# Optimization experiments

Measured on AMD Instinct MI355X. Metric: run time of the kernel, lower is better.

The kernel has to match this reference:

```python
import jax, jax.numpy as jnp
import numpy as np

B, IN, LAT, HID, OUT = 1024, 256, 512, 1024, 64
N_STEPS = 20          # fixed-step RK4 stand-in for adaptive odeint
T0, T1 = 0.0, 1.0     # integration interval from `time=(0.0, 1.0)`


def setup_inputs() -> dict:
    key = jax.random.key(0)
    ks = jax.random.split(key, 6)
    def glorot(k, shape):
        fan = shape[0]
        return (jax.random.normal(k, shape, jnp.float32) / np.float32(np.sqrt(fan)))
    return {
        "x": jax.random.normal(ks[0], (B, IN), jnp.float32),
        "W_in": glorot(ks[1], (IN, LAT)),
        "b_in": jnp.zeros((LAT,), jnp.float32),
        "W1": glorot(ks[2], (LAT + 1, HID)),   # +1 for the time column
        "b1": jnp.zeros((HID,), jnp.float32),
        "W2": glorot(ks[3], (HID, LAT)),
        "b2": jnp.zeros((LAT,), jnp.float32),
        "W_out": glorot(ks[4], (LAT // 2, OUT)),
        "b_out": jnp.zeros((OUT,), jnp.float32),
    }


def reference(x, W_in, b_in, W1, b1, W2, b2, W_out, b_out):
    # dynamics(inputs, time): concat scalar time as extra feature, run MLP
    def dyn(h, t):
        t_col = t * jnp.ones((h.shape[0], 1), h.dtype)
        z = jnp.concatenate([h, t_col], axis=-1)          # [B, LAT+1]
        return jnp.tanh(z @ W1 + b1) @ W2 + b2            # [B, LAT]

    # input_net: Dense + tanh
    h0 = jnp.tanh(x @ W_in + b_in)                        # [B, LAT]

    dt = jnp.float32((T1 - T0) / N_STEPS)
    ts = T0 + dt * jnp.arange(N_STEPS, dtype=jnp.float32)

    def rk4_step(h, t):
        k1 = dyn(h, t)
        k2 = dyn(h + 0.5 * dt * k1, t + 0.5 * dt)
        k3 = dyn(h + 0.5 * dt * k2, t + 0.5 * dt)
        k4 = dyn(h + dt * k3, t + dt)
        return h + (dt / 6.0) * (k1 + 2.0 * k2 + 2.0 * k3 + k4), None

    hT, _ = jax.lax.scan(rk4_step, h0, ts)                # latent at t=T1

    hidden = hT[:, : LAT // 2]                            # first half of latent
    out = hidden @ W_out + b_out                          # outputs head
    return out
```

## Files before the change

### kernel.cpp

```cpp
#include <hip/hip_runtime.h>
#include <hip/hip_bf16.h>

typedef __bf16 bf16x8 __attribute__((ext_vector_type(8)));
typedef __bf16 bf16x4 __attribute__((ext_vector_type(4)));
typedef float  f32x4  __attribute__((ext_vector_type(4)));

static constexpr int BB   = 1024;
static constexpr int INF  = 256;
static constexpr int LATF = 512;
static constexpr int HIDF = 1024;
static constexpr int OUTF = 64;
static constexpr float DT = 0.05f;

__device__ __forceinline__ void gload_lds16(const __bf16* g, __bf16* l) {
    __builtin_amdgcn_global_load_lds(
        (const __attribute__((address_space(1))) void*)g,
        (__attribute__((address_space(3))) void*)l, 16, 0, 0);
}

__device__ __forceinline__ void gload_lds16_x(const __bf16* g, __bf16* l, bool l2) {
    if (l2)
        __builtin_amdgcn_global_load_lds(
            (const __attribute__((address_space(1))) void*)g,
            (__attribute__((address_space(3))) void*)l, 16, 0, 1);
    else
        __builtin_amdgcn_global_load_lds(
            (const __attribute__((address_space(1))) void*)g,
            (__attribute__((address_space(3))) void*)l, 16, 0, 17);
}

__device__ __forceinline__ void store_bf16_x(__bf16* p, float v, bool l2) {
    const __bf16 b = (__bf16)v;
    unsigned u;
    __builtin_memcpy(&u, &b, 2);
    if (l2)
        asm volatile("global_store_short %0, %1, off sc0" :: "v"(p), "v"(u) : "memory");
    else
        asm volatile("global_store_short %0, %1, off sc0 sc1" :: "v"(p), "v"(u) : "memory");
}

__device__ __forceinline__ void drain_vmem() {
    asm volatile("s_waitcnt vmcnt(0)" ::: "memory");
}

__device__ __forceinline__ unsigned atomic_peek_l2(unsigned* p) {
    unsigned v, zero = 0;
    asm volatile("global_atomic_add %0, %1, %2, off sc0\n\ts_waitcnt vmcnt(0)"
                 : "=v"(v) : "v"(p), "v"(zero) : "memory");
    return v;
}

__device__ __forceinline__ void post_x(unsigned* p, bool l2) {
    if (l2) {
        unsigned one = 1u;
        asm volatile("global_atomic_add %0, %1, off" :: "v"(p), "v"(one) : "memory");
    } else {
        __hip_atomic_fetch_add(p, 1u, __ATOMIC_RELAXED, __HIP_MEMORY_SCOPE_AGENT);
    }
}

__device__ __forceinline__ void spin_ge_t0(unsigned* p, unsigned tgt, bool l2) {
    int guard = 0;
    if (l2) {
        while (atomic_peek_l2(p) < tgt) {
            __builtin_amdgcn_s_sleep(1);
            if (++guard > (1 << 16)) break;
        }
    } else {
        while (__hip_atomic_load(p, __ATOMIC_RELAXED, __HIP_MEMORY_SCOPE_AGENT) < tgt) {
            __builtin_amdgcn_s_sleep(1);
            if (++guard > (1 << 22)) break;
        }
    }
}

__device__ __forceinline__ float tanh_fast(float x) {
    float e = __expf(2.0f * x);
    return (e - 1.0f) / (e + 1.0f);
}

__global__ __launch_bounds__(256)
void prep_k(const float* __restrict__ x, __bf16* __restrict__ xb,
            const float* __restrict__ W_in, __bf16* __restrict__ WinT,
            const float* __restrict__ W1, __bf16* __restrict__ W1T,
            const float* __restrict__ W2, __bf16* __restrict__ W2T) {
    const int b = blockIdx.x;
    const int tx = threadIdx.x, ty = threadIdx.y;
    if (b < 256) {
        const int i = b * 256 + ty * 32 + tx;
        float4 v = reinterpret_cast<const float4*>(x)[i];
        bf16x4 o;
        o[0] = (__bf16)v.x; o[1] = (__bf16)v.y; o[2] = (__bf16)v.z; o[3] = (__bf16)v.w;
        reinterpret_cast<bf16x4*>(xb)[i] = o;
        return;
    }
    const float* src; __bf16* dst; int R, C, tb;
    if (b < 384)      { src = W_in; dst = WinT; R = 256;  C = 512;  tb = b - 256; }
    else if (b < 896) { src = W1;   dst = W1T;  R = 512;  C = 1024; tb = b - 384; }
    else              { src = W2;   dst = W2T;  R = 1024; C = 512;  tb = b - 896; }
    __shared__ float tile[32][33];
    const int nbc = C / 32;
    const int c0 = (tb % nbc) * 32, r0 = (tb / nbc) * 32;
#pragma unroll
    for (int i = 0; i < 32; i += 8)
        tile[ty + i][tx] = src[(size_t)(r0 + ty + i) * C + (c0 + tx)];
    __syncthreads();
#pragma unroll
    for (int i = 0; i < 32; i += 8)
        dst[(size_t)(c0 + ty + i) * R + (r0 + tx)] = (__bf16)tile[tx][ty + i];
}

__global__ __launch_bounds__(256, 1)
void ode_persist(const __bf16* __restrict__ xb, const __bf16* __restrict__ WinT,
                 const __bf16* __restrict__ W1T, const __bf16* __restrict__ W2T,
                 const float* __restrict__ b_in, const float* __restrict__ b1,
                 const float* __restrict__ wlast, const float* __restrict__ b2,
                 __bf16* __restrict__ zG, __bf16* __restrict__ gG,
                 float* __restrict__ hG, unsigned* __restrict__ flags) {
    __shared__ __align__(16) unsigned char SL[65536];
    __shared__ int sh_l2ok;

    const int bid   = blockIdx.x;
    const int rb    = (bid & 7) * 4 + ((bid >> 3) & 3);
    const int slice = bid >> 5;
    const int r0 = rb * 32;
    const int c1 = slice * 128;
    const int c2 = slice * 64;

    unsigned* czp = flags + rb * 32;
    unsigned* cgp = flags + rb * 32 + 16;

    const int tid  = threadIdx.x;
    const int w    = tid >> 6;
    const int lane = tid & 63;
    const int fr   = lane & 15;
    const int kq   = lane >> 4;
    const int cw   = w & 1;
    const int kw   = w >> 1;

    if (tid == 0) {
        unsigned* cvp   = flags + 1024;
        unsigned* cvp2  = flags + 1056;
        unsigned* trial = flags + 2048 + rb * 32;
        unsigned* vis   = flags + 4096;
        unsigned* okb   = flags + 12288;
        const unsigned magic = 0xC0DE0000u | (unsigned)bid;
        asm volatile("global_store_dword %0, %1, off sc0" :: "v"(&vis[bid * 32]), "v"(magic) : "memory");
        drain_vmem();
        __hip_atomic_fetch_add(cvp, 1u, __ATOMIC_RELAXED, __HIP_MEMORY_SCOPE_AGENT);
        { int g = 0; while (__hip_atomic_load(cvp, __ATOMIC_RELAXED, __HIP_MEMORY_SCOPE_AGENT) < 256u) { __builtin_amdgcn_s_sleep(1); if (++g > (1 << 22)) break; } }
        unsigned ok = 1;
        for (int s = 0; s < 8; ++s) {
            const int pb = (rb >> 2) + 8 * (rb & 3) + 32 * s;
            unsigned v;
            asm volatile("global_load_dword %0, %1, off sc0\n\ts_waitcnt vmcnt(0)"
                         : "=v"(v) : "v"(&vis[pb * 32]) : "memory");
            ok &= (v == (0xC0DE0000u | (unsigned)pb)) ? 1u : 0u;
        }
        {
            unsigned one = 1u;
            asm volatile("global_atomic_add %0, %1, off" :: "v"(trial), "v"(one) : "memory");
            int g = 0;
            while (atomic_peek_l2(trial) < 8u) {
                __builtin_amdgcn_s_sleep(1);
                if (++g > (1 << 15)) { ok = 0; break; }
            }
        }
        asm volatile("global_store_dword %0, %1, off sc0 sc1" :: "v"(&okb[bid * 32]), "v"(ok) : "memory");
        drain_vmem();
        __hip_atomic_fetch_add(cvp2, 1u, __ATOMIC_RELAXED, __HIP_MEMORY_SCOPE_AGENT);
        { int g = 0; while (__hip_atomic_load(cvp2, __ATOMIC_RELAXED, __HIP_MEMORY_SCOPE_AGENT) < 256u) { __builtin_amdgcn_s_sleep(1); if (++g > (1 << 22)) break; } }
        unsigned allok = 1;
        for (int s = 0; s < 8; ++s) {
            const int pb = (rb >> 2) + 8 * (rb & 3) + 32 * s;
            unsigned v;
            asm volatile("global_load_dword %0, %1, off sc0 sc1\n\ts_waitcnt vmcnt(0)"
                         : "=v"(v) : "v"(&okb[pb * 32]) : "memory");
            allok &= v;
        }
        sh_l2ok = (int)allok;
    }
    __syncthreads();
    const bool l2m = (sh_l2ok != 0);

    bf16x8 b1r[2][16];
#pragma unroll
    for (int n = 0; n < 2; ++n)
#pragma unroll
        for (int ks = 0; ks < 16; ++ks)
            b1r[n][ks] = *reinterpret_cast<const bf16x8*>(
                W1T + (size_t)(c1 + 32 * w + 16 * n + fr) * 512 + ks * 32 + kq * 8);

    bf16x8 b2r[2][16];
#pragma unroll
    for (int n = 0; n < 2; ++n)
#pragma unroll
        for (int ks = 0; ks < 16; ++ks)
            b2r[n][ks] = *reinterpret_cast<const bf16x8*>(
                W2T + (size_t)(c2 + 32 * cw + 16 * n + fr) * 1024 + kw * 512 + ks * 32 + kq * 8);

    float b1v[2], wlv[2], b2v[2], binv[2];
#pragma unroll
    for (int n = 0; n < 2; ++n) {
        const int colg = c1 + 32 * w + 16 * n + fr;
        b1v[n] = b1[colg];
        wlv[n] = wlast[colg];
        const int colk = c2 + 32 * cw + 16 * n + fr;
        b2v[n] = b2[colk];
        binv[n] = b_in[colk];
    }

    f32x4 hr[2][2], ha[2][2];

    {
#pragma unroll
        for (int i = 0; i < 4; ++i) {
            const int idx = w * 4 + i;
            const int row = idx * 2 + (lane >> 5);
            const int gam = (lane & 31) ^ (row & 7);
            gload_lds16(xb + (size_t)(r0 + row) * 256 + gam * 8,
                        (__bf16*)(SL + (size_t)idx * 1024));
        }
        bf16x8 winr[2][4];
#pragma unroll
        for (int n = 0; n < 2; ++n)
#pragma unroll
            for (int ks = 0; ks < 4; ++ks)
                winr[n][ks] = *reinterpret_cast<const bf16x8*>(
                    WinT + (size_t)(c2 + 32 * cw + 16 * n + fr) * 256 + kw * 128 + ks * 32 + kq * 8);
        __syncthreads();

        f32x4 acc[2][2];
#pragma unroll
        for (int mi = 0; mi < 2; ++mi)
#pragma unroll
            for (int n = 0; n < 2; ++n) acc[mi][n] = f32x4{0.f, 0.f, 0.f, 0.f};
#pragma unroll
        for (int ks = 0; ks < 4; ++ks) {
            bf16x8 a[2];
#pragma unroll
            for (int mi = 0; mi < 2; ++mi) {
                const int rowA = 16 * mi + fr;
                const int gk = kw * 16 + ks * 4 + kq;
                a[mi] = *reinterpret_cast<const bf16x8*>(
                    SL + (size_t)rowA * 512 + ((gk ^ (rowA & 7)) << 4));
            }
#pragma unroll
            for (int mi = 0; mi < 2; ++mi)
#pragma unroll
                for (int n = 0; n < 2; ++n)
                    acc[mi][n] = __builtin_amdgcn_mfma_f32_16x16x32_bf16(a[mi], winr[n][ks],
                                                                         acc[mi][n], 0, 0, 0);
        }
        __syncthreads();
        if (kw == 1) {
#pragma unroll
            for (int mi = 0; mi < 2; ++mi)
#pragma unroll
                for (int n = 0; n < 2; ++n)
                    *reinterpret_cast<f32x4*>(SL + cw * 4096 + ((mi * 2 + n) * 64 + lane) * 16) =
                        acc[mi][n];
        }
        __syncthreads();
        if (kw == 0) {
#pragma unroll
            for (int mi = 0; mi < 2; ++mi)
#pragma unroll
                for (int n = 0; n < 2; ++n) {
                    f32x4 part = *reinterpret_cast<const f32x4*>(
                        SL + cw * 4096 + ((mi * 2 + n) * 64 + lane) * 16);
#pragma unroll
                    for (int j = 0; j < 4; ++j) {
                        const float v = tanh_fast(acc[mi][n][j] + part[j] + binv[n]);
                        hr[mi][n][j] = v;
                        store_bf16_x(zG + (size_t)(r0 + 16 * mi + kq * 4 + j) * 512 +
                                          (c2 + 32 * cw + 16 * n + fr), v, l2m);
                    }
                }
        }
        drain_vmem();
        __syncthreads();
        if (tid == 0) post_x(czp, l2m);
    }

    for (int it = 0; it < 80; ++it) {
        const int s4 = it >> 2, st = it & 3;
        const float t = DT * (float)s4 + ((st == 0) ? 0.f : (st == 3) ? DT : 0.5f * DT);
        const unsigned tgt = 8u * (unsigned)(it + 1);

        if (tid == 0) spin_ge_t0(czp, tgt, l2m);
        __syncthreads();
#pragma unroll
        for (int i = 0; i < 8; ++i) {
            const int row = w * 8 + i;
            const int gam = lane ^ (row & 7);
            gload_lds16_x(zG + (size_t)(r0 + row) * 512 + gam * 8,
                          (__bf16*)(SL + (size_t)row * 1024), l2m);
        }
        __syncthreads();
        {
            f32x4 acc[2][2];
#pragma unroll
            for (int mi = 0; mi < 2; ++mi)
#pragma unroll
                for (int n = 0; n < 2; ++n) acc[mi][n] = f32x4{0.f, 0.f, 0.f, 0.f};
#pragma unroll
            for (int ks = 0; ks < 16; ++ks) {
                bf16x8 a[2];
#pragma unroll
                for (int mi = 0; mi < 2; ++mi) {
                    const int rowA = 16 * mi + fr;
                    const int gk = ks * 4 + kq;
                    a[mi] = *reinterpret_cast<const bf16x8*>(
                        SL + (size_t)rowA * 1024 + ((gk ^ (rowA & 7)) << 4));
                }
#pragma unroll
                for (int mi = 0; mi < 2; ++mi)
#pragma unroll
                    for (int n = 0; n < 2; ++n)
                        acc[mi][n] = __builtin_amdgcn_mfma_f32_16x16x32_bf16(a[mi], b1r[n][ks],
                                                                             acc[mi][n], 0, 0, 0);
            }
#pragma unroll
            for (int mi = 0; mi < 2; ++mi)
#pragma unroll
                for (int n = 0; n < 2; ++n)
#pragma unroll
                    for (int j = 0; j < 4; ++j) {
                        const float gv = tanh_fast(acc[mi][n][j] + b1v[n] + t * wlv[n]);
                        store_bf16_x(gG + (size_t)(r0 + 16 * mi + kq * 4 + j) * 1024 +
                                          (c1 + 32 * w + 16 * n + fr), gv, l2m);
                    }
        }
        drain_vmem();
        __syncthreads();
        if (tid == 0) {
            post_x(cgp, l2m);
            spin_ge_t0(cgp, tgt, l2m);
        }
        __syncthreads();
#pragma unroll
        for (int i = 0; i < 16; ++i) {
            const int idx = w * 16 + i;
            const int row = idx >> 1;
            const int p = ((idx & 1) << 6) | lane;
            const int gam = p ^ (row & 7);
            gload_lds16_x(gG + (size_t)(r0 + row) * 1024 + gam * 8,
                          (__bf16*)(SL + (size_t)idx * 1024), l2m);
        }
        __syncthreads();
        {
            f32x4 acc[2][2];
#pragma unroll
            for (int mi = 0; mi < 2; ++mi)
#pragma unroll
                for (int n = 0; n < 2; ++n) acc[mi][n] = f32x4{0.f, 0.f, 0.f, 0.f};
#pragma unroll
            for (int ks = 0; ks < 16; ++ks) {
                bf16x8 a[2];
#pragma unroll
                for (int mi = 0; mi < 2; ++mi) {
                    const int rowA = 16 * mi + fr;
                    const int gk = kw * 64 + ks * 4 + kq;
                    a[mi] = *reinterpret_cast<const bf16x8*>(
                        SL + (size_t)rowA * 2048 + ((gk ^ (rowA & 7)) << 4));
                }
#pragma unroll
                for (int mi = 0; mi < 2; ++mi)
#pragma unroll
                    for (int n = 0; n < 2; ++n)
                        acc[mi][n] = __builtin_amdgcn_mfma_f32_16x16x32_bf16(a[mi], b2r[n][ks],
                                                                             acc[mi][n], 0, 0, 0);
            }
            __syncthreads();
            if (kw == 1) {
#pragma unroll
                for (int mi = 0; mi < 2; ++mi)
#pragma unroll
                    for (int n = 0; n < 2; ++n)
                        *reinterpret_cast<f32x4*>(SL + cw * 4096 + ((mi * 2 + n) * 64 + lane) * 16) =
                            acc[mi][n];
            }
            __syncthreads();
            if (kw == 0) {
                const float wA = (st == 0 || st == 3) ? (DT / 6.0f) : (DT / 3.0f);
                const float cZ = (st < 2) ? (0.5f * DT) : DT;
#pragma unroll
                for (int mi = 0; mi < 2; ++mi)
#pragma unroll
                    for (int n = 0; n < 2; ++n) {
                        f32x4 part = *reinterpret_cast<const f32x4*>(
                            SL + cw * 4096 + ((mi * 2 + n) * 64 + lane) * 16);
#pragma unroll
                        for (int j = 0; j < 4; ++j) {
                            const float kv = acc[mi][n][j] + part[j] + b2v[n];
                            float zv;
                            if (st == 0) {
                                ha[mi][n][j] = hr[mi][n][j] + wA * kv;
                                zv = hr[mi][n][j] + cZ * kv;
                            } else if (st < 3) {
                                ha[mi][n][j] += wA * kv;
                                zv = hr[mi][n][j] + cZ * kv;
                            } else {
                                hr[mi][n][j] = ha[mi][n][j] + wA * kv;
                                zv = hr[mi][n][j];
                            }
                            store_bf16_x(zG + (size_t)(r0 + 16 * mi + kq * 4 + j) * 512 +
                                              (c2 + 32 * cw + 16 * n + fr), zv, l2m);
                        }
                    }
            }
        }
        drain_vmem();
        __syncthreads();
        if (tid == 0) post_x(czp, l2m);
    }

    if (kw == 0) {
#pragma unroll
        for (int mi = 0; mi < 2; ++mi)
#pragma unroll
            for (int n = 0; n < 2; ++n)
#pragma unroll
                for (int j = 0; j < 4; ++j)
                    hG[(size_t)(r0 + 16 * mi + kq * 4 + j) * 512 +
                       (c2 + 32 * cw + 16 * n + fr)] = hr[mi][n][j];
    }
}

__global__ __launch_bounds__(256)
void out_k(const float* __restrict__ h, const float* __restrict__ Wout,
           const float* __restrict__ bout, float* __restrict__ out) {
    const int col = threadIdx.x & 63;
    const int rg  = threadIdx.x >> 6;
    const int r0  = blockIdx.x * 16 + rg * 4;
    float a0 = 0.f, a1 = 0.f, a2 = 0.f, a3 = 0.f;
    for (int k = 0; k < 256; ++k) {
        const float w = Wout[k * OUTF + col];
        a0 += h[(r0 + 0) * LATF + k] * w;
        a1 += h[(r0 + 1) * LATF + k] * w;
        a2 += h[(r0 + 2) * LATF + k] * w;
        a3 += h[(r0 + 3) * LATF + k] * w;
    }
    const float b = bout[col];
    out[(r0 + 0) * OUTF + col] = a0 + b;
    out[(r0 + 1) * OUTF + col] = a1 + b;
    out[(r0 + 2) * OUTF + col] = a2 + b;
    out[(r0 + 3) * OUTF + col] = a3 + b;
}

extern "C" void kernel_launch(void* const* d_in, const int* in_sizes, int n_in,
                              void* d_out, int out_size, void* d_ws, size_t ws_size,
                              hipStream_t stream) {
    const float* x     = (const float*)d_in[0];
    const float* W_in  = (const float*)d_in[1];
    const float* b_in  = (const float*)d_in[2];
    const float* W1    = (const float*)d_in[3];
    const float* b1    = (const float*)d_in[4];
    const float* W2    = (const float*)d_in[5];
    const float* b2    = (const float*)d_in[6];
    const float* W_out = (const float*)d_in[7];
    const float* b_out = (const float*)d_in[8];
    float* out = (float*)d_out;

    char* ws = (char*)d_ws;
    size_t off = 0;
    auto alloc = [&](size_t bytes) {
        void* p = ws + off;
        off += (bytes + 255) & ~(size_t)255;
        return p;
    };
    __bf16* xb   = (__bf16*)alloc((size_t)BB * INF * 2);
    __bf16* WinT = (__bf16*)alloc((size_t)LATF * INF * 2);
    __bf16* W1T  = (__bf16*)alloc((size_t)HIDF * LATF * 2);
    __bf16* W2T  = (__bf16*)alloc((size_t)LATF * HIDF * 2);
    float*  h    = (float*)alloc((size_t)BB * LATF * 4);
    __bf16* zbuf = (__bf16*)alloc((size_t)BB * LATF * 2);
    __bf16* gbuf = (__bf16*)alloc((size_t)BB * HIDF * 2);
    unsigned* flags = (unsigned*)alloc(98304);
    if (off > ws_size) return;

    hipMemsetAsync(flags, 0, 98304, stream);
    prep_k<<<1408, dim3(32, 8), 0, stream>>>(x, xb, W_in, WinT, W1, W1T, W2, W2T);

    const float* w1last = W1 + (size_t)LATF * HIDF;

    ode_persist<<<256, 256, 0, stream>>>(xb, WinT, W1T, W2T, b_in, b1, w1last, b2,
                                         zbuf, gbuf, h, flags);

    out_k<<<BB / 16, 256, 0, stream>>>(h, W_out, b_out, out);
}
```

Baseline: 620.4 us.

## Split persistent ODE kernel into 512 blocks of 16 rows, two per CU

Halves the per-block row tile from 32 to 16 batch rows and doubles the persistent grid to 512 blocks, with launch bounds allowing two blocks per CU and LDS cut to fit. The block-to-row mapping, flag layout, co-residency checks and partner lists are reworked for the larger grid. The aim is more waves per CU to hide latency and shorter per-block critical paths between grid-wide syncs. In exchange each block holds all of its weight slice in registers for only half the rows, so per-row register and weight-load overhead doubles. It also adds register pressure under the tighter launch bound and more synchronisation participants.

```diff
diff --git a/kernel.cpp b/kernel.cpp
--- a/kernel.cpp
+++ b/kernel.cpp
@@ -110,20 +110,20 @@
         dst[(size_t)(c0 + ty + i) * R + (r0 + tx)] = (__bf16)tile[tx][ty + i];
 }
 
-__global__ __launch_bounds__(256, 1)
+__global__ __launch_bounds__(256, 2)
 void ode_persist(const __bf16* __restrict__ xb, const __bf16* __restrict__ WinT,
                  const __bf16* __restrict__ W1T, const __bf16* __restrict__ W2T,
                  const float* __restrict__ b_in, const float* __restrict__ b1,
                  const float* __restrict__ wlast, const float* __restrict__ b2,
                  __bf16* __restrict__ zG, __bf16* __restrict__ gG,
                  float* __restrict__ hG, unsigned* __restrict__ flags) {
-    __shared__ __align__(16) unsigned char SL[65536];
+    __shared__ __align__(16) unsigned char SL[36864];
     __shared__ int sh_l2ok;
 
     const int bid   = blockIdx.x;
-    const int rb    = (bid & 7) * 4 + ((bid >> 3) & 3);
-    const int slice = bid >> 5;
-    const int r0 = rb * 32;
+    const int rb    = (bid & 7) * 8 + ((bid >> 3) & 3) * 2 + (bid >> 8);
+    const int slice = (bid >> 5) & 7;
+    const int r0 = rb * 16;
     const int c1 = slice * 128;
     const int c2 = slice * 64;
 
@@ -139,19 +139,19 @@
     const int kw   = w >> 1;
 
     if (tid == 0) {
-        unsigned* cvp   = flags + 1024;
-        unsigned* cvp2  = flags + 1056;
-        unsigned* trial = flags + 2048 + rb * 32;
-        unsigned* vis   = flags + 4096;
-        unsigned* okb   = flags + 12288;
+        unsigned* cvp   = flags + 2048;
+        unsigned* cvp2  = flags + 2080;
+        unsigned* trial = flags + 4096 + rb * 32;
+        unsigned* vis   = flags + 8192;
+        unsigned* okb   = flags + 24576;
         const unsigned magic = 0xC0DE0000u | (unsigned)bid;
         asm volatile("global_store_dword %0, %1, off sc0" :: "v"(&vis[bid * 32]), "v"(magic) : "memory");
         drain_vmem();
         __hip_atomic_fetch_add(cvp, 1u, __ATOMIC_RELAXED, __HIP_MEMORY_SCOPE_AGENT);
-        { int g = 0; while (__hip_atomic_load(cvp, __ATOMIC_RELAXED, __HIP_MEMORY_SCOPE_AGENT) < 256u) { __builtin_amdgcn_s_sleep(1); if (++g > (1 << 22)) break; } }
+        { int g = 0; while (__hip_atomic_load(cvp, __ATOMIC_RELAXED, __HIP_MEMORY_SCOPE_AGENT) < 512u) { __builtin_amdgcn_s_sleep(1); if (++g > (1 << 22)) break; } }
         unsigned ok = 1;
         for (int s = 0; s < 8; ++s) {
-            const int pb = (rb >> 2) + 8 * (rb & 3) + 32 * s;
+            const int pb = (rb >> 3) | (((rb >> 1) & 3) << 3) | (s << 5) | ((rb & 1) << 8);
             unsigned v;
             asm volatile("global_load_dword %0, %1, off sc0\n\ts_waitcnt vmcnt(0)"
                          : "=v"(v) : "v"(&vis[pb * 32]) : "memory");
@@ -169,10 +169,10 @@
         asm volatile("global_store_dword %0, %1, off sc0 sc1" :: "v"(&okb[bid * 32]), "v"(ok) : "memory");
         drain_vmem();
         __hip_atomic_fetch_add(cvp2, 1u, __ATOMIC_RELAXED, __HIP_MEMORY_SCOPE_AGENT);
-        { int g = 0; while (__hip_atomic_load(cvp2, __ATOMIC_RELAXED, __HIP_MEMORY_SCOPE_AGENT) < 256u) { __builtin_amdgcn_s_sleep(1); if (++g > (1 << 22)) break; } }
+        { int g = 0; while (__hip_atomic_load(cvp2, __ATOMIC_RELAXED, __HIP_MEMORY_SCOPE_AGENT) < 512u) { __builtin_amdgcn_s_sleep(1); if (++g > (1 << 22)) break; } }
         unsigned allok = 1;
         for (int s = 0; s < 8; ++s) {
-            const int pb = (rb >> 2) + 8 * (rb & 3) + 32 * s;
+            const int pb = (rb >> 3) | (((rb >> 1) & 3) << 3) | (s << 5) | ((rb & 1) << 8);
             unsigned v;
             asm volatile("global_load_dword %0, %1, off sc0 sc1\n\ts_waitcnt vmcnt(0)"
                          : "=v"(v) : "v"(&okb[pb * 32]) : "memory");
@@ -210,12 +210,13 @@
         binv[n] = b_in[colk];
     }
 
-    f32x4 hr[2][2], ha[2][2];
+    f32x4 hr[2], ha[2];
+    unsigned char* SCR = SL + 32768;
 
     {
 #pragma unroll
-        for (int i = 0; i < 4; ++i) {
-            const int idx = w * 4 + i;
+        for (int i = 0; i < 2; ++i) {
+            const int idx = w * 2 + i;
             const int row = idx * 2 + (lane >> 5);
             const int gam = (lane & 31) ^ (row & 7);
             gload_lds16(xb + (size_t)(r0 + row) * 256 + gam * 8,
@@ -230,53 +231,37 @@
                     WinT + (size_t)(c2 + 32 * cw + 16 * n + fr) * 256 + kw * 128 + ks * 32 + kq * 8);
         __syncthreads();
 
-        f32x4 acc[2][2];
-#pragma unroll
-        for (int mi = 0; mi < 2; ++mi)
-#pragma unroll
-            for (int n = 0; n < 2; ++n) acc[mi][n] = f32x4{0.f, 0.f, 0.f, 0.f};
+        f32x4 acc[2];
+#pragma unroll
+        for (int n = 0; n < 2; ++n) acc[n] = f32x4{0.f, 0.f, 0.f, 0.f};
 #pragma unroll
         for (int ks = 0; ks < 4; ++ks) {
-            bf16x8 a[2];
-#pragma unroll
-            for (int mi = 0; mi < 2; ++mi) {
-                const int rowA = 16 * mi + fr;
-                const int gk = kw * 16 + ks * 4 + kq;
-                a[mi] = *reinterpret_cast<const bf16x8*>(
-                    SL + (size_t)rowA * 512 + ((gk ^ (rowA & 7)) << 4));
-            }
-#pragma unroll
-            for (int mi = 0; mi < 2; ++mi)
-#pragma unroll
-                for (int n = 0; n < 2; ++n)
-                    acc[mi][n] = __builtin_amdgcn_mfma_f32_16x16x32_bf16(a[mi], winr[n][ks],
-                                                                         acc[mi][n], 0, 0, 0);
+            const int gk = kw * 16 + ks * 4 + kq;
+            bf16x8 a = *reinterpret_cast<const bf16x8*>(
+                SL + (size_t)fr * 512 + ((gk ^ (fr & 7)) << 4));
+#pragma unroll
+            for (int n = 0; n < 2; ++n)
+                acc[n] = __builtin_amdgcn_mfma_f32_16x16x32_bf16(a, winr[n][ks], acc[n], 0, 0, 0);
         }
         __syncthreads();
         if (kw == 1) {
 #pragma unroll
-            for (int mi = 0; mi < 2; ++mi)
-#pragma unroll
-                for (int n = 0; n < 2; ++n)
-                    *reinterpret_cast<f32x4*>(SL + cw * 4096 + ((mi * 2 + n) * 64 + lane) * 16) =
-                        acc[mi][n];
+            for (int n = 0; n < 2; ++n)
+                *reinterpret_cast<f32x4*>(SCR + cw * 2048 + n * 1024 + lane * 16) = acc[n];
         }
         __syncthreads();
         if (kw == 0) {
 #pragma unroll
-            for (int mi = 0; mi < 2; ++mi)
-#pragma unroll
-                for (int n = 0; n < 2; ++n) {
-                    f32x4 part = *reinterpret_cast<const f32x4*>(
-                        SL + cw * 4096 + ((mi * 2 + n) * 64 + lane) * 16);
-#pragma unroll
-                    for (int j = 0; j < 4; ++j) {
-                        const float v = tanh_fast(acc[mi][n][j] + part[j] + binv[n]);
-                        hr[mi][n][j] = v;
-                        store_bf16_x(zG + (size_t)(r0 + 16 * mi + kq * 4 + j) * 512 +
-                                          (c2 + 32 * cw + 16 * n + fr), v, l2m);
-                    }
+            for (int n = 0; n < 2; ++n) {
+                f32x4 part = *reinterpret_cast<const f32x4*>(SCR + cw * 2048 + n * 1024 + lane * 16);
+#pragma unroll
+                for (int j = 0; j < 4; ++j) {
+                    const float v = tanh_fast(acc[n][j] + part[j] + binv[n]);
+                    hr[n][j] = v;
+                    store_bf16_x(zG + (size_t)(r0 + kq * 4 + j) * 512 +
+                                      (c2 + 32 * cw + 16 * n + fr), v, l2m);
                 }
+            }
         }
         drain_vmem();
         __syncthreads();
@@ -291,46 +276,34 @@
         if (tid == 0) spin_ge_t0(czp, tgt, l2m);
         __syncthreads();
 #pragma unroll
-        for (int i = 0; i < 8; ++i) {
-            const int row = w * 8 + i;
+        for (int i = 0; i < 4; ++i) {
+            const int row = w * 4 + i;
             const int gam = lane ^ (row & 7);
             gload_lds16_x(zG + (size_t)(r0 + row) * 512 + gam * 8,
                           (__bf16*)(SL + (size_t)row * 1024), l2m);
         }
         __syncthreads();
         {
-            f32x4 acc[2][2];
-#pragma unroll
-            for (int mi = 0; mi < 2; ++mi)
-#pragma unroll
-                for (int n = 0; n < 2; ++n) acc[mi][n] = f32x4{0.f, 0.f, 0.f, 0.f};
+            f32x4 acc[2];
+#pragma unroll
+            for (int n = 0; n < 2; ++n) acc[n] = f32x4{0.f, 0.f, 0.f, 0.f};
 #pragma unroll
             for (int ks = 0; ks < 16; ++ks) {
-                bf16x8 a[2];
-#pragma unroll
-                for (int mi = 0; mi < 2; ++mi) {
-                    const int rowA = 16 * mi + fr;
-                    const int gk = ks * 4 + kq;
-                    a[mi] = *reinterpret_cast<const bf16x8*>(
-                        SL + (size_t)rowA * 1024 + ((gk ^ (rowA & 7)) << 4));
+                const int gk = ks * 4 + kq;
+                bf16x8 a = *reinterpret_cast<const bf16x8*>(
+                    SL + (size_t)fr * 1024 + ((gk ^ (fr & 7)) << 4));
+#pragma unroll
+                for (int n = 0; n < 2; ++n)
+                    acc[n] = __builtin_amdgcn_mfma_f32_16x16x32_bf16(a, b1r[n][ks], acc[n], 0, 0, 0);
+            }
+#pragma unroll
+            for (int n = 0; n < 2; ++n)
+#pragma unroll
+                for (int j = 0; j < 4; ++j) {
+                    const float gv = tanh_fast(acc[n][j] + b1v[n] + t * wlv[n]);
+                    store_bf16_x(gG + (size_t)(r0 + kq * 4 + j) * 1024 +
+                                      (c1 + 32 * w + 16 * n + fr), gv, l2m);
                 }
-#pragma unroll
-                for (int mi = 0; mi < 2; ++mi)
-#pragma unroll
-                    for (int n = 0; n < 2; ++n)
-                        acc[mi][n] = __builtin_amdgcn_mfma_f32_16x16x32_bf16(a[mi], b1r[n][ks],
-                                                                             acc[mi][n], 0, 0, 0);
-            }
-#pragma unroll
-            for (int mi = 0; mi < 2; ++mi)
-#pragma unroll
-                for (int n = 0; n < 2; ++n)
-#pragma unroll
-                    for (int j = 0; j < 4; ++j) {
-                        const float gv = tanh_fast(acc[mi][n][j] + b1v[n] + t * wlv[n]);
-                        store_bf16_x(gG + (size_t)(r0 + 16 * mi + kq * 4 + j) * 1024 +
-                                          (c1 + 32 * w + 16 * n + fr), gv, l2m);
-                    }
         }
         drain_vmem();
         __syncthreads();
@@ -340,8 +313,8 @@
         }
         __syncthreads();
 #pragma unroll
-        for (int i = 0; i < 16; ++i) {
-            const int idx = w * 16 + i;
+        for (int i = 0; i < 8; ++i) {
+            const int idx = w * 8 + i;
             const int row = idx >> 1;
             const int p = ((idx & 1) << 6) | lane;
             const int gam = p ^ (row & 7);
@@ -350,65 +323,50 @@
         }
         __syncthreads();
         {
-            f32x4 acc[2][2];
-#pragma unroll
-            for (int mi = 0; mi < 2; ++mi)
-#pragma unroll
-                for (int n = 0; n < 2; ++n) acc[mi][n] = f32x4{0.f, 0.f, 0.f, 0.f};
+            f32x4 acc[2];
+#pragma unroll
+            for (int n = 0; n < 2; ++n) acc[n] = f32x4{0.f, 0.f, 0.f, 0.f};
 #pragma unroll
             for (int ks = 0; ks < 16; ++ks) {
-                bf16x8 a[2];
-#pragma unroll
-                for (int mi = 0; mi < 2; ++mi) {
-                    const int rowA = 16 * mi + fr;
-                    const int gk = kw * 64 + ks * 4 + kq;
-                    a[mi] = *reinterpret_cast<const bf16x8*>(
-                        SL + (size_t)rowA * 2048 + ((gk ^ (rowA & 7)) << 4));
-                }
-#pragma unroll
-                for (int mi = 0; mi < 2; ++mi)
-#pragma unroll
-                    for (int n = 0; n < 2; ++n)
-                        acc[mi][n] = __builtin_amdgcn_mfma_f32_16x16x32_bf16(a[mi], b2r[n][ks],
-                                                                             acc[mi][n], 0, 0, 0);
+                const int gk = kw * 64 + ks * 4 + kq;
+                bf16x8 a = *reinterpret_cast<const bf16x8*>(
+                    SL + (size_t)fr * 2048 + ((gk ^ (fr & 7)) << 4));
+#pragma unroll
+                for (int n = 0; n < 2; ++n)
+                    acc[n] = __builtin_amdgcn_mfma_f32_16x16x32_bf16(a, b2r[n][ks], acc[n], 0, 0, 0);
             }
             __syncthreads();
             if (kw == 1) {
 #pragma unroll
-                for (int mi = 0; mi < 2; ++mi)
-#pragma unroll
-                    for (int n = 0; n < 2; ++n)
-                        *reinterpret_cast<f32x4*>(SL + cw * 4096 + ((mi * 2 + n) * 64 + lane) * 16) =
-                            acc[mi][n];
+                for (int n = 0; n < 2; ++n)
+                    *reinterpret_cast<f32x4*>(SCR + cw * 2048 + n * 1024 + lane * 16) = acc[n];
             }
             __syncthreads();
             if (kw == 0) {
                 const float wA = (st == 0 || st == 3) ? (DT / 6.0f) : (DT / 3.0f);
                 const float cZ = (st < 2) ? (0.5f * DT) : DT;
 #pragma unroll
-                for (int mi = 0; mi < 2; ++mi)
-#pragma unroll
-                    for (int n = 0; n < 2; ++n) {
-                        f32x4 part = *reinterpret_cast<const f32x4*>(
-                            SL + cw * 4096 + ((mi * 2 + n) * 64 + lane) * 16);
-#pragma unroll
-                        for (int j = 0; j < 4; ++j) {
-                            const float kv = acc[mi][n][j] + part[j] + b2v[n];
-                            float zv;
-                            if (st == 0) {
-                                ha[mi][n][j] = hr[mi][n][j] + wA * kv;
-                                zv = hr[mi][n][j] + cZ * kv;
-                            } else if (st < 3) {
-                                ha[mi][n][j] += wA * kv;
-                                zv = hr[mi][n][j] + cZ * kv;
-                            } else {
-                                hr[mi][n][j] = ha[mi][n][j] + wA * kv;
-                                zv = hr[mi][n][j];
-                            }
-                            store_bf16_x(zG + (size_t)(r0 + 16 * mi + kq * 4 + j) * 512 +
-                                              (c2 + 32 * cw + 16 * n + fr), zv, l2m);
+                for (int n = 0; n < 2; ++n) {
+                    f32x4 part = *reinterpret_cast<const f32x4*>(
+                        SCR + cw * 2048 + n * 1024 + lane * 16);
+#pragma unroll
+                    for (int j = 0; j < 4; ++j) {
+                        const float kv = acc[n][j] + part[j] + b2v[n];
+                        float zv;
+                        if (st == 0) {
+                            ha[n][j] = hr[n][j] + wA * kv;
+                            zv = hr[n][j] + cZ * kv;
+                        } else if (st < 3) {
+                            ha[n][j] += wA * kv;
+                            zv = hr[n][j] + cZ * kv;
+                        } else {
+                            hr[n][j] = ha[n][j] + wA * kv;
+                            zv = hr[n][j];
                         }
+                        store_bf16_x(zG + (size_t)(r0 + kq * 4 + j) * 512 +
+                                          (c2 + 32 * cw + 16 * n + fr), zv, l2m);
                     }
+                }
             }
         }
         drain_vmem();
@@ -418,13 +376,11 @@
 
     if (kw == 0) {
 #pragma unroll
-        for (int mi = 0; mi < 2; ++mi)
-#pragma unroll
-            for (int n = 0; n < 2; ++n)
-#pragma unroll
-                for (int j = 0; j < 4; ++j)
-                    hG[(size_t)(r0 + 16 * mi + kq * 4 + j) * 512 +
-                       (c2 + 32 * cw + 16 * n + fr)] = hr[mi][n][j];
+        for (int n = 0; n < 2; ++n)
+#pragma unroll
+            for (int j = 0; j < 4; ++j)
+                hG[(size_t)(r0 + kq * 4 + j) * 512 +
+                   (c2 + 32 * cw + 16 * n + fr)] = hr[n][j];
     }
 }
 
@@ -477,15 +433,15 @@
     float*  h    = (float*)alloc((size_t)BB * LATF * 4);
     __bf16* zbuf = (__bf16*)alloc((size_t)BB * LATF * 2);
     __bf16* gbuf = (__bf16*)alloc((size_t)BB * HIDF * 2);
-    unsigned* flags = (unsigned*)alloc(98304);
+    unsigned* flags = (unsigned*)alloc(196608);
     if (off > ws_size) return;
 
-    hipMemsetAsync(flags, 0, 98304, stream);
+    hipMemsetAsync(flags, 0, 196608, stream);
     prep_k<<<1408, dim3(32, 8), 0, stream>>>(x, xb, W_in, WinT, W1, W1T, W2, W2T);
 
     const float* w1last = W1 + (size_t)LATF * HIDF;
 
-    ode_persist<<<256, 256, 0, stream>>>(xb, WinT, W1T, W2T, b_in, b1, w1last, b2,
+    ode_persist<<<512, 256, 0, stream>>>(xb, WinT, W1T, W2T, b_in, b1, w1last, b2,
                                          zbuf, gbuf, h, flags);
 
     out_k<<<BB / 16, 256, 0, stream>>>(h, W_out, b_out, out);
```

After: 1.581 ms. 155% more time.
